# Performance work log

Measured on AMD Instinct MI355X. Metric: run time of the kernel, lower is better.

## Reference

```python
import jax, jax.numpy as jnp
import numpy as np

W_IMG = 512
H_IMG = 512
D_MODEL = 192
N_FREQ = 8
LN_EPS = 1e-5


def _fourier_pe(coords_norm):
    # coords_norm: [B,K,2] in [0,1); returns [B,K,4*N_FREQ]
    freqs = 2.0 ** jnp.arange(N_FREQ, dtype=jnp.float32)  # [F]
    two_pi = 2.0 * jnp.pi
    x = coords_norm[..., 0:1] * freqs * two_pi  # [B,K,F]
    y = coords_norm[..., 1:2] * freqs * two_pi
    return jnp.concatenate([jnp.sin(x), jnp.cos(x), jnp.sin(y), jnp.cos(y)], axis=-1)


def _bilinear_sample(feat, gx, gy):
    # feat: [B,C,H,W]; gx,gy: [B,K] normalized coords in [-1,1], align_corners=True
    B, C, H, W = feat.shape
    ix = (gx + 1.0) * 0.5 * (W - 1)
    iy = (gy + 1.0) * 0.5 * (H - 1)
    ix0 = jnp.floor(ix)
    iy0 = jnp.floor(iy)
    wx = ix - ix0  # [B,K]
    wy = iy - iy0
    x0 = jnp.clip(ix0.astype(jnp.int32), 0, W - 1)
    x1 = jnp.clip(ix0.astype(jnp.int32) + 1, 0, W - 1)
    y0 = jnp.clip(iy0.astype(jnp.int32), 0, H - 1)
    y1 = jnp.clip(iy0.astype(jnp.int32) + 1, 0, H - 1)
    b = jnp.arange(B)[:, None]  # [B,1] broadcast against [B,K]
    g = lambda y, x: feat[b, :, y, x]  # [B,K,C]
    out = (g(y0, x0) * ((1 - wx) * (1 - wy))[..., None]
           + g(y0, x1) * (wx * (1 - wy))[..., None]
           + g(y1, x0) * ((1 - wx) * wy)[..., None]
           + g(y1, x1) * (wx * wy)[..., None])
    return out  # [B,K,C]


def setup_inputs() -> dict:
    key = jax.random.key(0)
    ks = jax.random.split(key, 16)
    B, K = 8, 4096
    # pixel coordinates in [0, W_IMG-1] x [0, H_IMG-1]
    u = jax.random.uniform(ks[0], (B, K, 2), dtype=jnp.float32)
    coords = u * jnp.array([W_IMG - 1, H_IMG - 1], dtype=jnp.float32)
    L1 = jax.random.normal(ks[1], (B, D_MODEL, 128, 128), dtype=jnp.float32)
    L2 = jax.random.normal(ks[2], (B, D_MODEL, 64, 64), dtype=jnp.float32)
    L3 = jax.random.normal(ks[3], (B, D_MODEL, 32, 32), dtype=jnp.float32)
    L4 = jax.random.normal(ks[4], (B, D_MODEL, 16, 16), dtype=jnp.float32)
    d_in = D_MODEL * 4 + 4 * N_FREQ  # 800
    Wseed_w = jax.random.normal(ks[5], (D_MODEL, d_in), dtype=jnp.float32) / np.sqrt(d_in)
    Wseed_b = jnp.zeros((D_MODEL,), dtype=jnp.float32)
    ln_g = jnp.ones((D_MODEL,), dtype=jnp.float32)
    ln_b = jnp.zeros((D_MODEL,), dtype=jnp.float32)
    Wpos_w = jax.random.normal(ks[6], (D_MODEL, 4 * N_FREQ), dtype=jnp.float32) / np.sqrt(4 * N_FREQ)
    Wpos_b = jnp.zeros((D_MODEL,), dtype=jnp.float32)
    return {"coords": coords, "L1": L1, "L2": L2, "L3": L3, "L4": L4,
            "Wseed_w": Wseed_w, "Wseed_b": Wseed_b, "ln_g": ln_g, "ln_b": ln_b,
            "Wpos_w": Wpos_w, "Wpos_b": Wpos_b}


def reference(coords, L1, L2, L3, L4, Wseed_w, Wseed_b, ln_g, ln_b, Wpos_w, Wpos_b):
    B, K, _ = coords.shape
    # normalized grid in [-1,1] (x uses W, y uses H), align_corners=True convention
    gx = 2.0 * coords[..., 0] / (W_IMG - 1) - 1.0  # [B,K]
    gy = 2.0 * coords[..., 1] / (H_IMG - 1) - 1.0
    center_grid = jnp.stack([gx, gy], axis=-1).reshape(B, K, 1, 2)
    coords_norm = coords / jnp.array([W_IMG, H_IMG], dtype=jnp.float32)
    pe_q = _fourier_pe(coords_norm)  # [B,K,32]
    f1 = _bilinear_sample(L1, gx, gy)
    f2 = _bilinear_sample(L2, gx, gy)
    f3 = _bilinear_sample(L3, gx, gy)
    f4 = _bilinear_sample(L4, gx, gy)
    x = jnp.concatenate([f1, f2, f3, f4, pe_q], axis=-1)  # [B,K,800]
    seed = x @ Wseed_w.T + Wseed_b
    mu = jnp.mean(seed, axis=-1, keepdims=True)
    var = jnp.mean((seed - mu) ** 2, axis=-1, keepdims=True)
    seed = (seed - mu) / jnp.sqrt(var + LN_EPS) * ln_g + ln_b
    pos = pe_q @ Wpos_w.T + Wpos_b
    return (seed, pos, center_grid)
```

## Files before the change

### kernel.cpp

```cpp
#include <hip/hip_runtime.h>
#include <hip/hip_bf16.h>
#include <stdint.h>

typedef unsigned short u16;
typedef short s16x8 __attribute__((ext_vector_type(8)));
typedef float f32x4 __attribute__((ext_vector_type(4)));
typedef uint32_t u32x4 __attribute__((ext_vector_type(4)));

__device__ __forceinline__ uint32_t pack_bf16(float lo, float hi) {
  float2 f; f.x = lo; f.y = hi;
  __hip_bfloat162 h = __float22bfloat162_rn(f);
  union { __hip_bfloat162 h; uint32_t u; } c; c.h = h;
  return c.u;
}
__device__ __forceinline__ u16 f2bf(float f) {
  union { float f; uint32_t u; } a; a.f = f;
  uint32_t u = a.u;
  return (u16)((u + 0x7fffu + ((u >> 16) & 1u)) >> 16);
}
__device__ __forceinline__ float bf2f(uint32_t hbits) {
  union { uint32_t u; float f; } a; a.u = hbits << 16;
  return a.f;
}

__global__ __launch_bounds__(256) void prep_all(
    const float* __restrict__ L1, const float* __restrict__ L2,
    const float* __restrict__ L3, const float* __restrict__ L4,
    const float* __restrict__ ws_w, const float* __restrict__ wp_w,
    u16* __restrict__ T1, u16* __restrict__ T2,
    u16* __restrict__ T3, u16* __restrict__ T4,
    u16* __restrict__ dWs, u16* __restrict__ dWp) {
  const int bid = blockIdx.x;
  const int t = threadIdx.x;

  if (bid >= 2720) {
    int t0 = (bid - 2720) * 256 + t;
    for (int i = t0; i < 39936; i += 8192) {
      const float* s; u16* d; int off;
      if (i < 38400) { s = ws_w; d = dWs; off = 4 * i; }
      else           { s = wp_w; d = dWp; off = 4 * (i - 38400); }
      f32x4 v = *(const f32x4*)(s + off);
      uint2 o;
      o.x = pack_bf16(v.x, v.y);
      o.y = pack_bf16(v.z, v.w);
      *(uint2*)(d + off) = o;
    }
    return;
  }

  const float* src; u16* dst; int HW, tiles, rel;
  if (bid < 2048)      { src = L1; dst = T1; HW = 16384; tiles = 256; rel = bid; }
  else if (bid < 2560) { src = L2; dst = T2; HW = 4096;  tiles = 64;  rel = bid - 2048; }
  else if (bid < 2688) { src = L3; dst = T3; HW = 1024;  tiles = 16;  rel = bid - 2560; }
  else                 { src = L4; dst = T4; HW = 256;   tiles = 4;   rel = bid - 2688; }
  const int b = rel / tiles, hw0 = (rel % tiles) * 64;

  __shared__ uint32_t tileD[96 * 65];
  const float* sb = src + (size_t)b * 192 * HW + hw0;
  for (int i = 0; i < 6; ++i) {
    int idx = i * 256 + t;
    int c2 = idx >> 4, hw4 = idx & 15;
    f32x4 a = *(const f32x4*)(sb + (size_t)(2 * c2) * HW + hw4 * 4);
    f32x4 c = *(const f32x4*)(sb + (size_t)(2 * c2 + 1) * HW + hw4 * 4);
    uint32_t* w = &tileD[c2 * 65 + hw4 * 4];
    w[0] = pack_bf16(a.x, c.x);
    w[1] = pack_bf16(a.y, c.y);
    w[2] = pack_bf16(a.z, c.z);
    w[3] = pack_bf16(a.w, c.w);
  }
  __syncthreads();
  uint32_t* d = (uint32_t*)(dst + ((size_t)b * HW + hw0) * 192);
  for (int i = 0; i < 12; ++i) {
    int e = i * 256 + t;
    int hw = e / 48, cp = e - hw * 48;
    uint2 v;
    v.x = tileD[(cp * 2) * 65 + hw];
    v.y = tileD[(cp * 2 + 1) * 65 + hw];
    *(uint2*)(d + hw * 96 + cp * 2) = v;
  }
}

__global__ __launch_bounds__(256, 3) void seed_main(
    const float* __restrict__ coords,
    const u16* __restrict__ T1, const u16* __restrict__ T2,
    const u16* __restrict__ T3, const u16* __restrict__ T4,
    const u16* __restrict__ Wseed, const u16* __restrict__ Wpos,
    const float* __restrict__ seed_b, const float* __restrict__ ln_g,
    const float* __restrict__ ln_b, const float* __restrict__ pos_b,
    float* __restrict__ out_seed, float* __restrict__ out_pos,
    float* __restrict__ out_cg) {

  __shared__ __align__(16) u16 xt[32 * 808];
  __shared__ float part_s[32][4], part_q[32][4];

  const int t = threadIdx.x;
  const int gp0 = blockIdx.x * 32;
  const int b = gp0 >> 12;

  if (t < 64) {
    int p = t >> 1, xy = t & 1;
    float c = coords[(gp0 + p) * 2 + xy];
    out_cg[(gp0 + p) * 2 + xy] = c * (2.0f / 511.0f) - 1.0f;
  }
  for (int i = 0; i < 4; ++i) {
    int e = i * 256 + t;
    int p = e >> 5, j = e & 31;
    float c = coords[(gp0 + p) * 2 + ((j >> 4) & 1)] * (1.0f / 512.0f);
    float v = c * (float)(1 << (j & 7));
    float a = (v - floorf(v)) * 6.283185307179586f;
    float r = (j & 8) ? __cosf(a) : __sinf(a);
    xt[p * 808 + 768 + j] = f2bf(r);
  }

  {
    const u16* B1 = T1 + (size_t)b * 16384 * 192;
    const u16* B2 = T2 + (size_t)b * 4096 * 192;
    const u16* B3 = T3 + (size_t)b * 1024 * 192;
    const u16* B4 = T4 + (size_t)b * 256 * 192;
    int plv = t >> 1;
    int lv = plv & 3, p = plv >> 2;
    int half = t & 1;
    float cx = coords[(gp0 + p) * 2 + 0];
    float cy = coords[(gp0 + p) * 2 + 1];
    float gx = cx * (2.0f / 511.0f) - 1.0f;
    float gy = cy * (2.0f / 511.0f) - 1.0f;
    int Wl = 128 >> lv;
    float ix = (gx + 1.0f) * 0.5f * (float)(Wl - 1);
    float iy = (gy + 1.0f) * 0.5f * (float)(Wl - 1);
    float fx = floorf(ix), fy = floorf(iy);
    float wx = ix - fx, wy = iy - fy;
    int x0 = (int)fx, y0 = (int)fy;
    int x1 = min(max(x0 + 1, 0), Wl - 1), y1 = min(max(y0 + 1, 0), Wl - 1);
    x0 = min(max(x0, 0), Wl - 1); y0 = min(max(y0, 0), Wl - 1);
    const u16* base = (lv == 0) ? B1 : (lv == 1) ? B2 : (lv == 2) ? B3 : B4;
    const u16* b00 = base + (y0 * Wl + x0) * 192 + half * 96;
    const u16* b01 = base + (y0 * Wl + x1) * 192 + half * 96;
    const u16* b10 = base + (y1 * Wl + x0) * 192 + half * 96;
    const u16* b11 = base + (y1 * Wl + x1) * 192 + half * 96;
    float w00 = (1.0f - wx) * (1.0f - wy), w01 = wx * (1.0f - wy);
    float w10 = (1.0f - wx) * wy,          w11 = wx * wy;
    u16* dstp = xt + p * 808 + lv * 192 + half * 96;
#pragma unroll
    for (int ii = 0; ii < 6; ++ii) {
      int ca = ii * 16, cb = ii * 16 + 8;
      u32x4 qa00 = *(const u32x4*)(b00 + ca), qb00 = *(const u32x4*)(b00 + cb);
      u32x4 qa01 = *(const u32x4*)(b01 + ca), qb01 = *(const u32x4*)(b01 + cb);
      u32x4 qa10 = *(const u32x4*)(b10 + ca), qb10 = *(const u32x4*)(b10 + cb);
      u32x4 qa11 = *(const u32x4*)(b11 + ca), qb11 = *(const u32x4*)(b11 + cb);
      u32x4 oa, ob;
#pragma unroll
      for (int k = 0; k < 4; ++k) {
        float lo = bf2f(qa00[k] & 0xffff) * w00 + bf2f(qa01[k] & 0xffff) * w01 +
                   bf2f(qa10[k] & 0xffff) * w10 + bf2f(qa11[k] & 0xffff) * w11;
        float hi = bf2f(qa00[k] >> 16) * w00 + bf2f(qa01[k] >> 16) * w01 +
                   bf2f(qa10[k] >> 16) * w10 + bf2f(qa11[k] >> 16) * w11;
        oa[k] = pack_bf16(lo, hi);
        lo = bf2f(qb00[k] & 0xffff) * w00 + bf2f(qb01[k] & 0xffff) * w01 +
             bf2f(qb10[k] & 0xffff) * w10 + bf2f(qb11[k] & 0xffff) * w11;
        hi = bf2f(qb00[k] >> 16) * w00 + bf2f(qb01[k] >> 16) * w01 +
             bf2f(qb10[k] >> 16) * w10 + bf2f(qb11[k] >> 16) * w11;
        ob[k] = pack_bf16(lo, hi);
      }
      *(u32x4*)(dstp + ca) = oa;
      *(u32x4*)(dstp + cb) = ob;
    }
  }
  __syncthreads();

  const int lid = t & 63, wv = t >> 6;
  const int quad = lid >> 4, mrow = lid & 15;
  const int nt0 = wv * 3;

  const u16* arow0 = xt + mrow * 808 + quad * 8;
  const u16* arow1 = arow0 + 16 * 808;
  const u16* w0 = Wseed + (size_t)((nt0 + 0) * 16 + mrow) * 800 + quad * 8;
  const u16* w1 = w0 + 16 * 800;
  const u16* w2 = w1 + 16 * 800;

  f32x4 accS[2][3];
#pragma unroll
  for (int mt = 0; mt < 2; ++mt)
#pragma unroll
    for (int j = 0; j < 3; ++j) accS[mt][j] = (f32x4)0.0f;

  s16x8 abuf[3][2], bbuf[3][3];
#pragma unroll
  for (int s = 0; s < 3; ++s) {
    int ko = s * 32;
    abuf[s][0] = *(const s16x8*)(arow0 + ko);
    abuf[s][1] = *(const s16x8*)(arow1 + ko);
    bbuf[s][0] = *(const s16x8*)(w0 + ko);
    bbuf[s][1] = *(const s16x8*)(w1 + ko);
    bbuf[s][2] = *(const s16x8*)(w2 + ko);
  }
#pragma unroll
  for (int kc = 0; kc < 25; ++kc) {
    const int cur = kc % 3;
    s16x8 a0 = abuf[cur][0], a1 = abuf[cur][1];
    s16x8 b0 = bbuf[cur][0], b1 = bbuf[cur][1], b2 = bbuf[cur][2];
    int nk = kc + 3;
    if (nk < 25) {
      int ko = nk * 32;
      abuf[cur][0] = *(const s16x8*)(arow0 + ko);
      abuf[cur][1] = *(const s16x8*)(arow1 + ko);
      bbuf[cur][0] = *(const s16x8*)(w0 + ko);
      bbuf[cur][1] = *(const s16x8*)(w1 + ko);
      bbuf[cur][2] = *(const s16x8*)(w2 + ko);
    }
    accS[0][0] = __builtin_amdgcn_mfma_f32_16x16x32_bf16(a0, b0, accS[0][0], 0, 0, 0);
    accS[1][0] = __builtin_amdgcn_mfma_f32_16x16x32_bf16(a1, b0, accS[1][0], 0, 0, 0);
    accS[0][1] = __builtin_amdgcn_mfma_f32_16x16x32_bf16(a0, b1, accS[0][1], 0, 0, 0);
    accS[1][1] = __builtin_amdgcn_mfma_f32_16x16x32_bf16(a1, b1, accS[1][1], 0, 0, 0);
    accS[0][2] = __builtin_amdgcn_mfma_f32_16x16x32_bf16(a0, b2, accS[0][2], 0, 0, 0);
    accS[1][2] = __builtin_amdgcn_mfma_f32_16x16x32_bf16(a1, b2, accS[1][2], 0, 0, 0);
  }

  {
    s16x8 ap0 = *(const s16x8*)(arow0 + 768);
    s16x8 ap1 = *(const s16x8*)(arow1 + 768);
#pragma unroll
    for (int j = 0; j < 3; ++j) {
      int n = (nt0 + j) * 16 + mrow;
      s16x8 bw = *(const s16x8*)(Wpos + n * 32 + quad * 8);
      f32x4 p0 = (f32x4)0.0f, p1 = (f32x4)0.0f;
      p0 = __builtin_amdgcn_mfma_f32_16x16x32_bf16(ap0, bw, p0, 0, 0, 0);
      p1 = __builtin_amdgcn_mfma_f32_16x16x32_bf16(ap1, bw, p1, 0, 0, 0);
      float pb = pos_b[n];
#pragma unroll
      for (int r = 0; r < 4; ++r) {
        out_pos[(size_t)(gp0 + quad * 4 + r) * 192 + n] = p0[r] + pb;
        out_pos[(size_t)(gp0 + 16 + quad * 4 + r) * 192 + n] = p1[r] + pb;
      }
    }
  }

#pragma unroll
  for (int j = 0; j < 3; ++j) {
    float sb = seed_b[(nt0 + j) * 16 + mrow];
#pragma unroll
    for (int mt = 0; mt < 2; ++mt)
#pragma unroll
      for (int r = 0; r < 4; ++r) accS[mt][j][r] += sb;
  }
#pragma unroll
  for (int mt = 0; mt < 2; ++mt)
#pragma unroll
    for (int r = 0; r < 4; ++r) {
      float s = accS[mt][0][r] + accS[mt][1][r] + accS[mt][2][r];
      float q = accS[mt][0][r] * accS[mt][0][r] + accS[mt][1][r] * accS[mt][1][r] +
                accS[mt][2][r] * accS[mt][2][r];
#pragma unroll
      for (int d = 1; d < 16; d <<= 1) {
        s += __shfl_xor(s, d, 16);
        q += __shfl_xor(q, d, 16);
      }
      if (mrow == 0) {
        int row = mt * 16 + quad * 4 + r;
        part_s[row][wv] = s;
        part_q[row][wv] = q;
      }
    }
  __syncthreads();

#pragma unroll
  for (int mt = 0; mt < 2; ++mt) {
    float mu[4], rs[4];
#pragma unroll
    for (int r = 0; r < 4; ++r) {
      int row = mt * 16 + quad * 4 + r;
      float s = part_s[row][0] + part_s[row][1] + part_s[row][2] + part_s[row][3];
      float q = part_q[row][0] + part_q[row][1] + part_q[row][2] + part_q[row][3];
      float m = s * (1.0f / 192.0f);
      float var = q * (1.0f / 192.0f) - m * m;
      mu[r] = m;
      rs[r] = rsqrtf(var + 1e-5f);
    }
#pragma unroll
    for (int j = 0; j < 3; ++j) {
      int n = (nt0 + j) * 16 + mrow;
      float g = ln_g[n], bb = ln_b[n];
#pragma unroll
      for (int r = 0; r < 4; ++r) {
        int row = gp0 + mt * 16 + quad * 4 + r;
        out_seed[(size_t)row * 192 + n] = (accS[mt][j][r] - mu[r]) * rs[r] * g + bb;
      }
    }
  }
}

extern "C" void kernel_launch(void* const* d_in, const int* in_sizes, int n_in,
                              void* d_out, int out_size, void* d_ws, size_t ws_size,
                              hipStream_t stream) {
  const float* coords  = (const float*)d_in[0];
  const float* L1      = (const float*)d_in[1];
  const float* L2      = (const float*)d_in[2];
  const float* L3      = (const float*)d_in[3];
  const float* L4      = (const float*)d_in[4];
  const float* Wseed_w = (const float*)d_in[5];
  const float* Wseed_b = (const float*)d_in[6];
  const float* ln_g    = (const float*)d_in[7];
  const float* ln_b    = (const float*)d_in[8];
  const float* Wpos_w  = (const float*)d_in[9];
  const float* Wpos_b  = (const float*)d_in[10];

  u16* T1  = (u16*)d_ws;
  u16* T2  = T1 + (size_t)8 * 16384 * 192;
  u16* T3  = T2 + (size_t)8 * 4096 * 192;
  u16* T4  = T3 + (size_t)8 * 1024 * 192;
  u16* Wsd = T4 + (size_t)8 * 256 * 192;
  u16* Wps = Wsd + 153600;

  prep_all<<<2752, 256, 0, stream>>>(L1, L2, L3, L4, Wseed_w, Wpos_w,
                                     T1, T2, T3, T4, Wsd, Wps);

  float* out_seed = (float*)d_out;
  float* out_pos  = out_seed + (size_t)32768 * 192;
  float* out_cg   = out_pos  + (size_t)32768 * 192;

  seed_main<<<1024, 256, 0, stream>>>(coords, T1, T2, T3, T4, Wsd, Wps,
                                      Wseed_b, ln_g, ln_b, Wpos_b,
                                      out_seed, out_pos, out_cg);
}
```

Baseline: 279.5 us.

## Split gather and GEMM into separate kernels with async LDS staging

```diff
diff --git a/kernel.cpp b/kernel.cpp
--- a/kernel.cpp
+++ b/kernel.cpp
@@ -6,6 +6,14 @@
 typedef short s16x8 __attribute__((ext_vector_type(8)));
 typedef float f32x4 __attribute__((ext_vector_type(4)));
 typedef uint32_t u32x4 __attribute__((ext_vector_type(4)));
+
+#define GLOBAL_AS __attribute__((address_space(1)))
+#define LDS_AS    __attribute__((address_space(3)))
+
+__device__ __forceinline__ void async_copy16(const void* g, void* l) {
+  __builtin_amdgcn_global_load_lds((const GLOBAL_AS uint32_t*)g,
+                                   (LDS_AS uint32_t*)l, 16, 0, 0);
+}
 
 __device__ __forceinline__ uint32_t pack_bf16(float lo, float hi) {
   float2 f; f.x = lo; f.y = hi;
@@ -80,89 +88,112 @@
   }
 }
 
-__global__ __launch_bounds__(256, 3) void seed_main(
+__global__ __launch_bounds__(256, 3) void gather_kernel(
     const float* __restrict__ coords,
     const u16* __restrict__ T1, const u16* __restrict__ T2,
     const u16* __restrict__ T3, const u16* __restrict__ T4,
+    u16* __restrict__ xg, float* __restrict__ out_cg) {
+  const int g = blockIdx.x * 256 + threadIdx.x;
+  const int p = g >> 4;
+  const int sub = g & 15, lv = sub >> 2, q = sub & 3;
+  const int b = p >> 12;
+
+  const float cx = coords[p * 2 + 0];
+  const float cy = coords[p * 2 + 1];
+  const float gx = cx * (2.0f / 511.0f) - 1.0f;
+  const float gy = cy * (2.0f / 511.0f) - 1.0f;
+  const int Wl = 128 >> lv;
+  float ix = (gx + 1.0f) * 0.5f * (float)(Wl - 1);
+  float iy = (gy + 1.0f) * 0.5f * (float)(Wl - 1);
+  float fx = floorf(ix), fy = floorf(iy);
+  float wx = ix - fx, wy = iy - fy;
+  int x0 = (int)fx, y0 = (int)fy;
+  int x1 = min(max(x0 + 1, 0), Wl - 1), y1 = min(max(y0 + 1, 0), Wl - 1);
+  x0 = min(max(x0, 0), Wl - 1); y0 = min(max(y0, 0), Wl - 1);
+
+  const u16* base =
+      (lv == 0) ? T1 + (size_t)b * 16384 * 192 :
+      (lv == 1) ? T2 + (size_t)b * 4096 * 192 :
+      (lv == 2) ? T3 + (size_t)b * 1024 * 192 :
+                  T4 + (size_t)b * 256 * 192;
+  const u16* b00 = base + (y0 * Wl + x0) * 192 + q * 48;
+  const u16* b01 = base + (y0 * Wl + x1) * 192 + q * 48;
+  const u16* b10 = base + (y1 * Wl + x0) * 192 + q * 48;
+  const u16* b11 = base + (y1 * Wl + x1) * 192 + q * 48;
+
+  u32x4 r00[6], r01[6], r10[6], r11[6];
+#pragma unroll
+  for (int i = 0; i < 6; ++i) r00[i] = *(const u32x4*)(b00 + i * 8);
+#pragma unroll
+  for (int i = 0; i < 6; ++i) r01[i] = *(const u32x4*)(b01 + i * 8);
+#pragma unroll
+  for (int i = 0; i < 6; ++i) r10[i] = *(const u32x4*)(b10 + i * 8);
+#pragma unroll
+  for (int i = 0; i < 6; ++i) r11[i] = *(const u32x4*)(b11 + i * 8);
+
+  if (lv == 0 && q == 0) {
+    out_cg[p * 2 + 0] = gx;
+    out_cg[p * 2 + 1] = gy;
+  }
+  if (lv == 3) {
+    uint32_t pe[4];
+#pragma unroll
+    for (int h = 0; h < 4; ++h) {
+      float r2[2];
+#pragma unroll
+      for (int k = 0; k < 2; ++k) {
+        int j = q * 8 + h * 2 + k;
+        float c = ((j >> 4) & 1) ? cy : cx;
+        float v = c * (1.0f / 512.0f) * (float)(1 << (j & 7));
+        float a = (v - floorf(v)) * 6.283185307179586f;
+        r2[k] = (j & 8) ? __cosf(a) : __sinf(a);
+      }
+      pe[h] = pack_bf16(r2[0], r2[1]);
+    }
+    *(u32x4*)(xg + (size_t)p * 808 + 768 + q * 8) =
+        *(u32x4*)pe;
+  }
+
+  const float w00 = (1.0f - wx) * (1.0f - wy), w01 = wx * (1.0f - wy);
+  const float w10 = (1.0f - wx) * wy,          w11 = wx * wy;
+  u16* dst = xg + (size_t)p * 808 + lv * 192 + q * 48;
+#pragma unroll
+  for (int i = 0; i < 6; ++i) {
+    u32x4 o;
+#pragma unroll
+    for (int k = 0; k < 4; ++k) {
+      float lo = bf2f(r00[i][k] & 0xffff) * w00 + bf2f(r01[i][k] & 0xffff) * w01 +
+                 bf2f(r10[i][k] & 0xffff) * w10 + bf2f(r11[i][k] & 0xffff) * w11;
+      float hi = bf2f(r00[i][k] >> 16) * w00 + bf2f(r01[i][k] >> 16) * w01 +
+                 bf2f(r10[i][k] >> 16) * w10 + bf2f(r11[i][k] >> 16) * w11;
+      o[k] = pack_bf16(lo, hi);
+    }
+    *(u32x4*)(dst + i * 8) = o;
+  }
+}
+
+__global__ __launch_bounds__(256, 3) void gemm_kernel(
+    const u16* __restrict__ xg,
     const u16* __restrict__ Wseed, const u16* __restrict__ Wpos,
     const float* __restrict__ seed_b, const float* __restrict__ ln_g,
     const float* __restrict__ ln_b, const float* __restrict__ pos_b,
-    float* __restrict__ out_seed, float* __restrict__ out_pos,
-    float* __restrict__ out_cg) {
+    float* __restrict__ out_seed, float* __restrict__ out_pos) {
 
   __shared__ __align__(16) u16 xt[32 * 808];
   __shared__ float part_s[32][4], part_q[32][4];
 
   const int t = threadIdx.x;
   const int gp0 = blockIdx.x * 32;
-  const int b = gp0 >> 12;
-
-  if (t < 64) {
-    int p = t >> 1, xy = t & 1;
-    float c = coords[(gp0 + p) * 2 + xy];
-    out_cg[(gp0 + p) * 2 + xy] = c * (2.0f / 511.0f) - 1.0f;
-  }
-  for (int i = 0; i < 4; ++i) {
-    int e = i * 256 + t;
-    int p = e >> 5, j = e & 31;
-    float c = coords[(gp0 + p) * 2 + ((j >> 4) & 1)] * (1.0f / 512.0f);
-    float v = c * (float)(1 << (j & 7));
-    float a = (v - floorf(v)) * 6.283185307179586f;
-    float r = (j & 8) ? __cosf(a) : __sinf(a);
-    xt[p * 808 + 768 + j] = f2bf(r);
-  }
 
   {
-    const u16* B1 = T1 + (size_t)b * 16384 * 192;
-    const u16* B2 = T2 + (size_t)b * 4096 * 192;
-    const u16* B3 = T3 + (size_t)b * 1024 * 192;
-    const u16* B4 = T4 + (size_t)b * 256 * 192;
-    int plv = t >> 1;
-    int lv = plv & 3, p = plv >> 2;
-    int half = t & 1;
-    float cx = coords[(gp0 + p) * 2 + 0];
-    float cy = coords[(gp0 + p) * 2 + 1];
-    float gx = cx * (2.0f / 511.0f) - 1.0f;
-    float gy = cy * (2.0f / 511.0f) - 1.0f;
-    int Wl = 128 >> lv;
-    float ix = (gx + 1.0f) * 0.5f * (float)(Wl - 1);
-    float iy = (gy + 1.0f) * 0.5f * (float)(Wl - 1);
-    float fx = floorf(ix), fy = floorf(iy);
-    float wx = ix - fx, wy = iy - fy;
-    int x0 = (int)fx, y0 = (int)fy;
-    int x1 = min(max(x0 + 1, 0), Wl - 1), y1 = min(max(y0 + 1, 0), Wl - 1);
-    x0 = min(max(x0, 0), Wl - 1); y0 = min(max(y0, 0), Wl - 1);
-    const u16* base = (lv == 0) ? B1 : (lv == 1) ? B2 : (lv == 2) ? B3 : B4;
-    const u16* b00 = base + (y0 * Wl + x0) * 192 + half * 96;
-    const u16* b01 = base + (y0 * Wl + x1) * 192 + half * 96;
-    const u16* b10 = base + (y1 * Wl + x0) * 192 + half * 96;
-    const u16* b11 = base + (y1 * Wl + x1) * 192 + half * 96;
-    float w00 = (1.0f - wx) * (1.0f - wy), w01 = wx * (1.0f - wy);
-    float w10 = (1.0f - wx) * wy,          w11 = wx * wy;
-    u16* dstp = xt + p * 808 + lv * 192 + half * 96;
-#pragma unroll
-    for (int ii = 0; ii < 6; ++ii) {
-      int ca = ii * 16, cb = ii * 16 + 8;
-      u32x4 qa00 = *(const u32x4*)(b00 + ca), qb00 = *(const u32x4*)(b00 + cb);
-      u32x4 qa01 = *(const u32x4*)(b01 + ca), qb01 = *(const u32x4*)(b01 + cb);
-      u32x4 qa10 = *(const u32x4*)(b10 + ca), qb10 = *(const u32x4*)(b10 + cb);
-      u32x4 qa11 = *(const u32x4*)(b11 + ca), qb11 = *(const u32x4*)(b11 + cb);
-      u32x4 oa, ob;
-#pragma unroll
-      for (int k = 0; k < 4; ++k) {
-        float lo = bf2f(qa00[k] & 0xffff) * w00 + bf2f(qa01[k] & 0xffff) * w01 +
-                   bf2f(qa10[k] & 0xffff) * w10 + bf2f(qa11[k] & 0xffff) * w11;
-        float hi = bf2f(qa00[k] >> 16) * w00 + bf2f(qa01[k] >> 16) * w01 +
-                   bf2f(qa10[k] >> 16) * w10 + bf2f(qa11[k] >> 16) * w11;
-        oa[k] = pack_bf16(lo, hi);
-        lo = bf2f(qb00[k] & 0xffff) * w00 + bf2f(qb01[k] & 0xffff) * w01 +
-             bf2f(qb10[k] & 0xffff) * w10 + bf2f(qb11[k] & 0xffff) * w11;
-        hi = bf2f(qb00[k] >> 16) * w00 + bf2f(qb01[k] >> 16) * w01 +
-             bf2f(qb10[k] >> 16) * w10 + bf2f(qb11[k] >> 16) * w11;
-        ob[k] = pack_bf16(lo, hi);
-      }
-      *(u32x4*)(dstp + ca) = oa;
-      *(u32x4*)(dstp + cb) = ob;
+    const char* src = (const char*)(xg + (size_t)gp0 * 808);
+    char* ldst = (char*)xt;
+#pragma unroll
+    for (int r = 0; r < 13; ++r) {
+      if (r < 12 || t < 160) {
+        int off = r * 4096 + t * 16;
+        async_copy16(src + off, ldst + off);
+      }
     }
   }
   __syncthreads();
@@ -309,6 +340,7 @@
   u16* T4  = T3 + (size_t)8 * 1024 * 192;
   u16* Wsd = T4 + (size_t)8 * 256 * 192;
   u16* Wps = Wsd + 153600;
+  u16* xg  = Wps + 6144;
 
   prep_all<<<2752, 256, 0, stream>>>(L1, L2, L3, L4, Wseed_w, Wpos_w,
                                      T1, T2, T3, T4, Wsd, Wps);
@@ -317,7 +349,8 @@
   float* out_pos  = out_seed + (size_t)32768 * 192;
   float* out_cg   = out_pos  + (size_t)32768 * 192;
 
-  seed_main<<<1024, 256, 0, stream>>>(coords, T1, T2, T3, T4, Wsd, Wps,
-                                      Wseed_b, ln_g, ln_b, Wpos_b,
-                                      out_seed, out_pos, out_cg);
-}
+  gather_kernel<<<2048, 256, 0, stream>>>(coords, T1, T2, T3, T4, xg, out_cg);
+
+  gemm_kernel<<<1024, 256, 0, stream>>>(xg, Wsd, Wps, Wseed_b, ln_g, ln_b,
+                                        Wpos_b, out_seed, out_pos);
+}
```

Result: no change. 283.2 us (+1.4%).
